# Kernel optimization log

Measured on AMD Instinct MI355X. Metric: run time of the kernel, lower is better.

The kernel has to match this reference:

```python
import jax, jax.numpy as jnp
import numpy as np

N, E, G, DIN, DH = 50000, 800000, 256, 128, 128
BN_EPS = 1e-5


def _gin_layer(h, src, dst, W1, b1, gamma, beta, W2, b2):
    # GINConv (eps=0): agg_i = sum_{(j->i) in edges} h_j ; z = agg + h
    agg = jnp.zeros_like(h).at[dst].add(h[src])
    z = agg + h
    z = z @ W1 + b1
    # BatchNorm1d (training mode: batch stats over nodes, biased var)
    mean = z.mean(axis=0)
    var = z.var(axis=0)
    z = gamma * (z - mean) * jax.lax.rsqrt(var + BN_EPS) + beta
    z = jax.nn.relu(z)
    z = z @ W2 + b2
    return jax.nn.relu(z)


def setup_inputs() -> dict:
    key = jax.random.key(0)
    ks = jax.random.split(key, 12)
    x = jax.random.normal(ks[0], (N, DIN), dtype=jnp.float32)
    edge_index = jax.random.randint(ks[1], (2, E), 0, N, dtype=jnp.int32)
    batch = jnp.sort(jax.random.randint(ks[2], (N,), 0, G, dtype=jnp.int32))
    s = 0.05
    W1 = jax.random.normal(ks[3], (7, DIN, DH), dtype=jnp.float32) * s
    b1 = jnp.zeros((7, DH), dtype=jnp.float32)
    gamma = jnp.ones((7, DH), dtype=jnp.float32)
    beta = jnp.zeros((7, DH), dtype=jnp.float32)
    W2 = jax.random.normal(ks[4], (7, DH, DH), dtype=jnp.float32) * s
    b2 = jnp.zeros((7, DH), dtype=jnp.float32)
    Wl1 = jax.random.normal(ks[5], (14 * DH, 14 * DH), dtype=jnp.float32) * s
    bl1 = jnp.zeros((14 * DH,), dtype=jnp.float32)
    Wl2 = jax.random.normal(ks[6], (14 * DH, 1), dtype=jnp.float32) * s
    bl2 = jnp.zeros((1,), dtype=jnp.float32)
    return {"x": x, "edge_index": edge_index, "batch": batch,
            "W1": W1, "b1": b1, "gamma": gamma, "beta": beta,
            "W2": W2, "b2": b2, "Wl1": Wl1, "bl1": bl1,
            "Wl2": Wl2, "bl2": bl2}


def reference(x, edge_index, batch, W1, b1, gamma, beta, W2, b2, Wl1, bl1, Wl2, bl2):
    src, dst = edge_index[0], edge_index[1]
    hs = []
    h = x
    for i in range(7):
        h = _gin_layer(h, src, dst, W1[i], b1[i], gamma[i], beta[i], W2[i], b2[i])
        hs.append(h)
    adds = [jax.ops.segment_sum(hi, batch, num_segments=G) for hi in hs]
    maxs = [jax.ops.segment_max(hi, batch, num_segments=G) for hi in hs]
    h = jnp.concatenate(adds + maxs, axis=1)  # [G, 14*DH]
    h = jax.nn.relu(h @ Wl1 + bl1)
    h = h @ Wl2 + bl2
    return (jax.nn.sigmoid(h), h)
```

## Files before the change

### kernel.cpp

```cpp
#include <hip/hip_runtime.h>
#include <cstdint>
#include <cstddef>

#define NN 50000
#define NE 800000
#define NG 256
#define NLAY 7
#define NBLK 782
#define CAP 18432

typedef float f32x4 __attribute__((ext_vector_type(4)));
typedef __bf16 bf16x8 __attribute__((ext_vector_type(8)));
typedef _Float16 h16x8 __attribute__((ext_vector_type(8)));

__device__ __forceinline__ float4 ld4(const float* p) { return *(const float4*)p; }
__device__ __forceinline__ void addh8(float4& x, float4& y, h16x8 v) {
  x.x += (float)v[0]; x.y += (float)v[1]; x.z += (float)v[2]; x.w += (float)v[3];
  y.x += (float)v[4]; y.y += (float)v[5]; y.z += (float)v[6]; y.w += (float)v[7];
}

__global__ void k_init(const float* __restrict__ x, const float* __restrict__ W1,
                       const float* __restrict__ W2, int* __restrict__ counts,
                       int* __restrict__ gcur, float* __restrict__ pooled,
                       _Float16* __restrict__ hb,
                       __bf16* __restrict__ w1f, __bf16* __restrict__ w2f) {
  int i = blockIdx.x * 256 + threadIdx.x;
  if (i < NN) counts[i] = 0;
  if (i < 49) gcur[i] = i * CAP;
  if (i < NG * 1792) pooled[i] = 0.f;
  if (i < NN * 128) hb[i] = (_Float16)x[i];
  if (i < NLAY * 32768) {
    int l = i >> 15, pos = i & 32767;
    int j = pos & 7, ln = (pos >> 3) & 63, slot = (pos >> 9) & 15, kc = pos >> 13;
    int hl = slot & 1, ctp = (slot >> 1) & 3, hfp = slot >> 3;
    int n = hfp * 64 + ctp * 16 + (ln & 15);
    int k = kc * 32 + ((ln >> 4) << 3) + j;
    float a = W1[l * 16384 + k * 128 + n];
    float b = W2[l * 16384 + k * 128 + n];
    __bf16 ah = (__bf16)a, bh = (__bf16)b;
    w1f[i] = hl ? (__bf16)(a - (float)ah) : ah;
    w2f[i] = hl ? (__bf16)(b - (float)bh) : bh;
  }
}

__global__ void k_hist(const int* __restrict__ edge, int* __restrict__ counts) {
  int e = blockIdx.x * 256 + threadIdx.x;
  if (e < NE) atomicAdd(&counts[edge[NE + e]], 1);
}

__global__ void k_part(const int* __restrict__ counts, int* __restrict__ bsum) {
  __shared__ int sm[256];
  int b = blockIdx.x, t = threadIdx.x;
  int i = b * 256 + t;
  sm[t] = (i < NN) ? counts[i] : 0;
  __syncthreads();
  for (int s = 128; s > 0; s >>= 1) {
    if (t < s) sm[t] += sm[t + s];
    __syncthreads();
  }
  if (t == 0) bsum[b] = sm[0];
}

__global__ void k_bscan(const int* __restrict__ bsum, int* __restrict__ boff,
                        int* __restrict__ row_ptr) {
  __shared__ int sm[256];
  int t = threadIdx.x;
  int v = (t < 196) ? bsum[t] : 0;
  sm[t] = v;
  __syncthreads();
  int val = v;
  for (int off = 1; off < 256; off <<= 1) {
    int o = (t >= off) ? sm[t - off] : 0;
    __syncthreads();
    val += o;
    sm[t] = val;
    __syncthreads();
  }
  if (t < 196) boff[t] = val - v;
  if (t == 255) row_ptr[NN] = val;
}

__global__ void k_rowptr(const int* __restrict__ counts, const int* __restrict__ boff,
                         int* __restrict__ row_ptr) {
  __shared__ int sm[256];
  int b = blockIdx.x, t = threadIdx.x;
  int i = b * 256 + t;
  int c = (i < NN) ? counts[i] : 0;
  sm[t] = c;
  __syncthreads();
  int val = c;
  for (int off = 1; off < 256; off <<= 1) {
    int o = (t >= off) ? sm[t - off] : 0;
    __syncthreads();
    val += o;
    sm[t] = val;
    __syncthreads();
  }
  if (i < NN) row_ptr[i] = val - c + boff[b];
}

__global__ __launch_bounds__(256) void k_binA(const int* __restrict__ edge,
                                              int* __restrict__ gcur,
                                              unsigned int* __restrict__ bins) {
  __shared__ int lh[49], lbase[49], lt[49];
  const int tid = threadIdx.x;
  const int e0 = blockIdx.x * 3125, e1 = e0 + 3125;
  if (tid < 49) { lh[tid] = 0; lt[tid] = 0; }
  __syncthreads();
  for (int e = e0 + tid; e < e1; e += 256)
    atomicAdd(&lh[edge[NE + e] >> 10], 1);
  __syncthreads();
  if (tid < 49) lbase[tid] = atomicAdd(&gcur[tid], lh[tid]);
  __syncthreads();
  for (int e = e0 + tid; e < e1; e += 256) {
    int dst = edge[NE + e], src = edge[e];
    int r = dst >> 10;
    int t = atomicAdd(&lt[r], 1);
    bins[lbase[r] + t] = ((unsigned)dst << 16) | (unsigned)src;
  }
}

__global__ __launch_bounds__(512) void k_binB(const int* __restrict__ row_ptr,
                                              const int* __restrict__ gcur,
                                              const unsigned int* __restrict__ bins,
                                              unsigned short* __restrict__ csr16) {
  __shared__ int lcur[1024];
  __shared__ unsigned short lcsr[24576];
  const int blk = blockIdx.x, tid = threadIdx.x;
  const int base = blk << 10;
  const int nn = (base + 1024 <= NN) ? 1024 : (NN - base);
  const int seg0 = row_ptr[base];
  const int seg1 = row_ptr[(base + 1024 <= NN) ? (base + 1024) : NN];
  for (int i = tid; i < nn; i += 512) lcur[i] = row_ptr[base + i] - seg0;
  __syncthreads();
  const int tot = gcur[blk] - blk * CAP;
  for (int t = tid; t < tot; t += 512) {
    unsigned int p = bins[blk * CAP + t];
    int dst = (int)(p >> 16), src = (int)(p & 0xffffu);
    int pos = atomicAdd(&lcur[dst - base], 1);
    lcsr[pos] = (unsigned short)src;
  }
  __syncthreads();
  for (int i = tid; i < seg1 - seg0; i += 512) csr16[seg0 + i] = lcsr[i];
}

__device__ __forceinline__ void split8(const float4 v0, const float4 v1,
                                       bf16x8& hi, bf16x8& lo) {
  float f[8] = {v0.x, v0.y, v0.z, v0.w, v1.x, v1.y, v1.z, v1.w};
  #pragma unroll
  for (int j = 0; j < 8; ++j) {
    __bf16 h = (__bf16)f[j];
    hi[j] = h;
    lo[j] = (__bf16)(f[j] - (float)h);
  }
}

__device__ __forceinline__ void mfma_phase(
    int tid, const __bf16* __restrict__ wf, float (*zs)[132], f32x4 acc[4])
{
  const int wv = tid >> 6, stripe = wv >> 1, half = wv & 1;
  const int lane = tid & 63, q = lane >> 4, m = lane & 15;
  #pragma unroll
  for (int kc = 0; kc < 4; ++kc) {
    const int k0 = kc * 32 + q * 8;
    float4 v0 = *(const float4*)&zs[stripe * 16 + m][k0];
    float4 v1 = *(const float4*)&zs[stripe * 16 + m][k0 + 4];
    bf16x8 ah, al;
    split8(v0, v1, ah, al);
    #pragma unroll
    for (int ct = 0; ct < 4; ++ct) {
      const int sbase = (half * 4 + ct) * 2;
      const __bf16* bp = wf + (((size_t)(kc * 16 + sbase) * 64 + lane) << 3);
      bf16x8 bh = *(const bf16x8*)bp;
      bf16x8 bl = *(const bf16x8*)(bp + 512);
      acc[ct] = __builtin_amdgcn_mfma_f32_16x16x32_bf16(ah, bh, acc[ct], 0, 0, 0);
      acc[ct] = __builtin_amdgcn_mfma_f32_16x16x32_bf16(ah, bl, acc[ct], 0, 0, 0);
      acc[ct] = __builtin_amdgcn_mfma_f32_16x16x32_bf16(al, bh, acc[ct], 0, 0, 0);
    }
  }
  __syncthreads();
}

__global__ __launch_bounds__(512) void k_fused1(
    const _Float16* __restrict__ hb, const int* __restrict__ row_ptr,
    const unsigned short* __restrict__ csr_src, const __bf16* __restrict__ wf,
    const float* __restrict__ bias, _Float16* __restrict__ zb,
    float* __restrict__ psum, float* __restrict__ psq)
{
  __shared__ float zs[64][132];
  const int tid = threadIdx.x;
  const int m0 = blockIdx.x * 64;

  {
    const int lr = tid >> 3;
    const int sub = tid & 7;
    const int r = m0 + lr;
    const int c0 = sub << 4;
    float4 a0 = make_float4(0,0,0,0), a1 = a0, a2 = a0, a3 = a0;
    float4 b0 = a0, b1 = a0, b2 = a0, b3 = a0;
    if (r < NN) {
      const _Float16* hp = hb + ((size_t)r << 7) + c0;
      addh8(a0, a1, *(const h16x8*)hp);
      addh8(a2, a3, *(const h16x8*)(hp + 8));
      int e = row_ptr[r], e1 = row_ptr[r + 1];
      for (; e + 3 < e1; e += 4) {
        const _Float16* p0 = hb + ((size_t)csr_src[e] << 7) + c0;
        const _Float16* p1 = hb + ((size_t)csr_src[e + 1] << 7) + c0;
        const _Float16* p2 = hb + ((size_t)csr_src[e + 2] << 7) + c0;
        const _Float16* p3 = hb + ((size_t)csr_src[e + 3] << 7) + c0;
        h16x8 v0a = *(const h16x8*)p0, v0b = *(const h16x8*)(p0 + 8);
        h16x8 v1a = *(const h16x8*)p1, v1b = *(const h16x8*)(p1 + 8);
        h16x8 v2a = *(const h16x8*)p2, v2b = *(const h16x8*)(p2 + 8);
        h16x8 v3a = *(const h16x8*)p3, v3b = *(const h16x8*)(p3 + 8);
        addh8(a0, a1, v0a); addh8(a2, a3, v0b);
        addh8(b0, b1, v1a); addh8(b2, b3, v1b);
        addh8(a0, a1, v2a); addh8(a2, a3, v2b);
        addh8(b0, b1, v3a); addh8(b2, b3, v3b);
      }
      for (; e < e1; ++e) {
        const _Float16* p0 = hb + ((size_t)csr_src[e] << 7) + c0;
        addh8(a0, a1, *(const h16x8*)p0);
        addh8(a2, a3, *(const h16x8*)(p0 + 8));
      }
      a0.x += b0.x; a0.y += b0.y; a0.z += b0.z; a0.w += b0.w;
      a1.x += b1.x; a1.y += b1.y; a1.z += b1.z; a1.w += b1.w;
      a2.x += b2.x; a2.y += b2.y; a2.z += b2.z; a2.w += b2.w;
      a3.x += b3.x; a3.y += b3.y; a3.z += b3.z; a3.w += b3.w;
    }
    *(float4*)&zs[lr][c0 + 0] = a0;
    *(float4*)&zs[lr][c0 + 4] = a1;
    *(float4*)&zs[lr][c0 + 8] = a2;
    *(float4*)&zs[lr][c0 + 12] = a3;
  }
  __syncthreads();

  const int wv = tid >> 6, stripe = wv >> 1, half = wv & 1;
  const int lane = tid & 63, q = lane >> 4, m = lane & 15;
  f32x4 acc[4] = {};
  mfma_phase(tid, wf, zs, acc);

  float* red_s = (float*)zs;
  float* red_q = red_s + 2176;
  const int sl = stripe * 4 + q;
  #pragma unroll
  for (int ct = 0; ct < 4; ++ct) {
    const int col = half * 64 + ct * 16 + m;
    const float bb = bias[col];
    float s = 0.f, qq = 0.f;
    #pragma unroll
    for (int i = 0; i < 4; ++i) {
      int r = m0 + stripe * 16 + q * 4 + i;
      if (r < NN) {
        float o = acc[ct][i] + bb;
        zb[((size_t)r << 7) + col] = (_Float16)o;
        s += o; qq += o * o;
      }
    }
    red_s[col * 17 + sl] = s;
    red_q[col * 17 + sl] = qq;
  }
  __syncthreads();
  if (tid < 128) {
    float s = 0.f, qq = 0.f;
    #pragma unroll
    for (int k = 0; k < 16; ++k) {
      s += red_s[tid * 17 + k];
      qq += red_q[tid * 17 + k];
    }
    psum[blockIdx.x * 128 + tid] = s;
    psq[blockIdx.x * 128 + tid] = qq;
  }
}

__global__ __launch_bounds__(256) void k_bnfin(
    const float* __restrict__ psum, const float* __restrict__ psq,
    const float* __restrict__ gamma, const float* __restrict__ beta,
    float* __restrict__ ab) {
  __shared__ float ss[256], sq[256];
  int col = blockIdx.x;
  int t = threadIdx.x;
  float s = 0.f, q = 0.f;
  for (int b = t; b < NBLK; b += 256) {
    s += psum[b * 128 + col];
    q += psq[b * 128 + col];
  }
  ss[t] = s; sq[t] = q;
  __syncthreads();
  for (int st = 128; st > 0; st >>= 1) {
    if (t < st) { ss[t] += ss[t + st]; sq[t] += sq[t + st]; }
    __syncthreads();
  }
  if (t == 0) {
    float mean = ss[0] * (1.f / NN);
    float var = sq[0] * (1.f / NN) - mean * mean;
    float rstd = rsqrtf(var + 1e-5f);
    float a = gamma[col] * rstd;
    ab[col] = a;
    ab[128 + col] = beta[col] - mean * a;
  }
}

__global__ __launch_bounds__(512) void k_fused2(
    const _Float16* __restrict__ zb, const float* __restrict__ ab,
    const __bf16* __restrict__ wf, const float* __restrict__ bias,
    _Float16* __restrict__ hb, const int* __restrict__ batch,
    float* __restrict__ pooled, int layer)
{
  __shared__ float zs[64][132];
  const int tid = threadIdx.x;
  const int m0 = blockIdx.x * 64;

  {
    const int lr = tid >> 3;
    const int sub = tid & 7;
    const int r = m0 + lr;
    const int c0 = sub << 4;
    h16x8 u0 = {}, u1 = {};
    if (r < NN) {
      const _Float16* rp = zb + ((size_t)r << 7) + c0;
      u0 = *(const h16x8*)rp;
      u1 = *(const h16x8*)(rp + 8);
    }
    float4 v0 = make_float4((float)u0[0], (float)u0[1], (float)u0[2], (float)u0[3]);
    float4 v1 = make_float4((float)u0[4], (float)u0[5], (float)u0[6], (float)u0[7]);
    float4 v2 = make_float4((float)u1[0], (float)u1[1], (float)u1[2], (float)u1[3]);
    float4 v3 = make_float4((float)u1[4], (float)u1[5], (float)u1[6], (float)u1[7]);
    float4 s0 = ld4(ab + c0), s1 = ld4(ab + c0 + 4);
    float4 s2 = ld4(ab + c0 + 8), s3 = ld4(ab + c0 + 12);
    float4 o0 = ld4(ab + 128 + c0), o1 = ld4(ab + 128 + c0 + 4);
    float4 o2 = ld4(ab + 128 + c0 + 8), o3 = ld4(ab + 128 + c0 + 12);
    float4 y0, y1, y2, y3;
    y0.x = fmaxf(fmaf(s0.x, v0.x, o0.x), 0.f); y0.y = fmaxf(fmaf(s0.y, v0.y, o0.y), 0.f);
    y0.z = fmaxf(fmaf(s0.z, v0.z, o0.z), 0.f); y0.w = fmaxf(fmaf(s0.w, v0.w, o0.w), 0.f);
    y1.x = fmaxf(fmaf(s1.x, v1.x, o1.x), 0.f); y1.y = fmaxf(fmaf(s1.y, v1.y, o1.y), 0.f);
    y1.z = fmaxf(fmaf(s1.z, v1.z, o1.z), 0.f); y1.w = fmaxf(fmaf(s1.w, v1.w, o1.w), 0.f);
    y2.x = fmaxf(fmaf(s2.x, v2.x, o2.x), 0.f); y2.y = fmaxf(fmaf(s2.y, v2.y, o2.y), 0.f);
    y2.z = fmaxf(fmaf(s2.z, v2.z, o2.z), 0.f); y2.w = fmaxf(fmaf(s2.w, v2.w, o2.w), 0.f);
    y3.x = fmaxf(fmaf(s3.x, v3.x, o3.x), 0.f); y3.y = fmaxf(fmaf(s3.y, v3.y, o3.y), 0.f);
    y3.z = fmaxf(fmaf(s3.z, v3.z, o3.z), 0.f); y3.w = fmaxf(fmaf(s3.w, v3.w, o3.w), 0.f);
    *(float4*)&zs[lr][c0 + 0] = y0;
    *(float4*)&zs[lr][c0 + 4] = y1;
    *(float4*)&zs[lr][c0 + 8] = y2;
    *(float4*)&zs[lr][c0 + 12] = y3;
  }
  __syncthreads();

  const int wv = tid >> 6, stripe = wv >> 1, half = wv & 1;
  const int lane = tid & 63, q = lane >> 4, m = lane & 15;
  f32x4 acc[4] = {};
  mfma_phase(tid, wf, zs, acc);

  int bg[4];
  #pragma unroll
  for (int i = 0; i < 4; ++i) {
    int r = m0 + stripe * 16 + q * 4 + i;
    bg[i] = (r < NN) ? batch[r] : -1;
  }
  #pragma unroll
  for (int ct = 0; ct < 4; ++ct) {
    const int col = half * 64 + ct * 16 + m;
    const float bb = bias[col];
    #pragma unroll
    for (int i = 0; i < 4; ++i) {
      int r = m0 + stripe * 16 + q * 4 + i;
      float v = fmaxf(acc[ct][i] + bb, 0.f);
      acc[ct][i] = v;
      if (r < NN) hb[((size_t)r << 7) + col] = (_Float16)v;
    }
  }

  int gstart = batch[m0];
  int gend = batch[(m0 + 63 < NN) ? (m0 + 63) : (NN - 1)];
  float* red_s = (float*)zs;
  float* red_m = red_s + 2176;
  const int sl = stripe * 4 + q;
  for (int g = gstart; g <= gend; ++g) {
    __syncthreads();
    #pragma unroll
    for (int ct = 0; ct < 4; ++ct) {
      const int col = half * 64 + ct * 16 + m;
      float s = 0.f, mx = 0.f;
      #pragma unroll
      for (int i = 0; i < 4; ++i) {
        if (bg[i] == g) { s += acc[ct][i]; mx = fmaxf(mx, acc[ct][i]); }
      }
      red_s[col * 17 + sl] = s;
      red_m[col * 17 + sl] = mx;
    }
    __syncthreads();
    if (tid < 128) {
      float s = 0.f, mx = 0.f;
      #pragma unroll
      for (int k = 0; k < 16; ++k) {
        s += red_s[tid * 17 + k];
        mx = fmaxf(mx, red_m[tid * 17 + k]);
      }
      if (s != 0.f) atomicAdd(&pooled[g * 1792 + layer * 128 + tid], s);
      if (mx != 0.f)
        atomicMax((int*)&pooled[g * 1792 + 896 + layer * 128 + tid], __float_as_int(mx));
    }
  }
}

__global__ __launch_bounds__(256) void k_wl1prep(
    const float* __restrict__ Wl1, __bf16* __restrict__ wh, __bf16* __restrict__ wl) {
  __shared__ float tile[32][33];
  const int k0 = blockIdx.x * 32, n0 = blockIdx.y * 32;
  const int lr = threadIdx.x >> 5, lc = threadIdx.x & 31;
  #pragma unroll
  for (int it = 0; it < 4; ++it) {
    int rr = lr + it * 8;
    tile[rr][lc] = Wl1[(size_t)(k0 + rr) * 1792 + n0 + lc];
  }
  __syncthreads();
  #pragma unroll
  for (int it = 0; it < 4; ++it) {
    int rr = lr + it * 8;
    float v = tile[lc][rr];
    __bf16 h = (__bf16)v;
    wh[(size_t)(n0 + rr) * 1792 + k0 + lc] = h;
    wl[(size_t)(n0 + rr) * 1792 + k0 + lc] = (__bf16)(v - (float)h);
  }
}

__global__ __launch_bounds__(256) void k_mlp1a(
    const float* __restrict__ P, const __bf16* __restrict__ wh,
    const __bf16* __restrict__ wl, float* __restrict__ part)
{
  const int tid = threadIdx.x;
  const int n0 = blockIdx.x * 64;
  const int m0 = blockIdx.y * 64;
  const int kc = blockIdx.z;
  const int kbase = kc * 448;
  const int w = tid >> 6, lane = tid & 63, q = lane >> 4, m = lane & 15;
  const int row = m0 + w * 16 + m;
  f32x4 acc[4] = {};
  const float* rp = P + (size_t)row * 1792;
  #pragma unroll 2
  for (int ks = 0; ks < 14; ++ks) {
    const int k0 = kbase + ks * 32 + q * 8;
    float4 v0 = ld4(rp + k0), v1 = ld4(rp + k0 + 4);
    bf16x8 ah, al;
    split8(v0, v1, ah, al);
    #pragma unroll
    for (int ct = 0; ct < 4; ++ct) {
      const int n = n0 + ct * 16 + m;
      bf16x8 bh = *(const bf16x8*)(wh + (size_t)n * 1792 + k0);
      bf16x8 bl = *(const bf16x8*)(wl + (size_t)n * 1792 + k0);
      acc[ct] = __builtin_amdgcn_mfma_f32_16x16x32_bf16(ah, bh, acc[ct], 0, 0, 0);
      acc[ct] = __builtin_amdgcn_mfma_f32_16x16x32_bf16(ah, bl, acc[ct], 0, 0, 0);
      acc[ct] = __builtin_amdgcn_mfma_f32_16x16x32_bf16(al, bh, acc[ct], 0, 0, 0);
    }
  }
  float* pp = part + (size_t)kc * 458752;
  #pragma unroll
  for (int ct = 0; ct < 4; ++ct) {
    const int n = n0 + ct * 16 + m;
    #pragma unroll
    for (int i = 0; i < 4; ++i) {
      int r = m0 + w * 16 + q * 4 + i;
      pp[(size_t)r * 1792 + n] = acc[ct][i];
    }
  }
}

__global__ void k_mlp2(const float* __restrict__ part, const float* __restrict__ bl1,
                       const float* __restrict__ Wl2, const float* __restrict__ bl2,
                       float* __restrict__ out) {
  __shared__ float red[256];
  int g = blockIdx.x, t = threadIdx.x;
  float p = 0.f;
  for (int k = t; k < 1792; k += 256) {
    size_t idx = (size_t)g * 1792 + k;
    float s = bl1[k];
    #pragma unroll
    for (int kc = 0; kc < 4; ++kc) s += part[(size_t)kc * 458752 + idx];
    p += fmaxf(s, 0.f) * Wl2[k];
  }
  red[t] = p;
  __syncthreads();
  for (int s = 128; s > 0; s >>= 1) {
    if (t < s) red[t] += red[t + s];
    __syncthreads();
  }
  if (t == 0) {
    float l = red[0] + bl2[0];
    out[g] = 1.f / (1.f + expf(-l));
    out[NG + g] = l;
  }
}

extern "C" void kernel_launch(void* const* d_in, const int* in_sizes, int n_in,
                              void* d_out, int out_size, void* d_ws, size_t ws_size,
                              hipStream_t stream) {
  const float* x     = (const float*)d_in[0];
  const int*   edge  = (const int*)d_in[1];
  const int*   batch = (const int*)d_in[2];
  const float* W1    = (const float*)d_in[3];
  const float* b1    = (const float*)d_in[4];
  const float* gamma = (const float*)d_in[5];
  const float* beta  = (const float*)d_in[6];
  const float* W2    = (const float*)d_in[7];
  const float* b2    = (const float*)d_in[8];
  const float* Wl1   = (const float*)d_in[9];
  const float* bl1   = (const float*)d_in[10];
  const float* Wl2   = (const float*)d_in[11];
  const float* bl2   = (const float*)d_in[12];
  float* out = (float*)d_out;

  int* wsi = (int*)d_ws;
  int* row_ptr = wsi;
  int* counts  = wsi + 50048;
  int* bsum    = wsi + 100096;
  int* boff    = wsi + 100352;
  int* gcur    = wsi + 100608;
  unsigned short* csr16 = (unsigned short*)(wsi + 100864);
  float* wsf   = (float*)(wsi + 950912);
  _Float16* zb     = (_Float16*)wsf;
  _Float16* hb     = (_Float16*)(wsf + 6400000);
  float*    part   = wsf + 9600000;
  float*    psum   = wsf + 12800000;
  float*    psq    = wsf + 12900096;
  float*    ab     = wsf + 13000192;
  float*    pooled = wsf + 13000448;
  __bf16*   w1f    = (__bf16*)(wsf + 13459200);
  __bf16*   w2f    = (__bf16*)(wsf + 13573888);
  unsigned int* bins = (unsigned int*)wsf;
  __bf16*   wl1h   = (__bf16*)wsf;
  __bf16*   wl1l   = (__bf16*)(wsf + 1605632);

  k_init<<<25000, 256, 0, stream>>>(x, W1, W2, counts, gcur, pooled, hb, w1f, w2f);
  k_hist<<<3125, 256, 0, stream>>>(edge, counts);
  k_part<<<196, 256, 0, stream>>>(counts, bsum);
  k_bscan<<<1, 256, 0, stream>>>(bsum, boff, row_ptr);
  k_rowptr<<<196, 256, 0, stream>>>(counts, boff, row_ptr);
  k_binA<<<256, 256, 0, stream>>>(edge, gcur, bins);
  k_binB<<<49, 512, 0, stream>>>(row_ptr, gcur, bins, csr16);

  for (int i = 0; i < NLAY; ++i) {
    k_fused1<<<NBLK, 512, 0, stream>>>(hb, row_ptr, csr16, w1f + i * 32768,
                                       b1 + i * 128, zb, psum, psq);
    k_bnfin<<<128, 256, 0, stream>>>(psum, psq, gamma + i * 128, beta + i * 128, ab);
    k_fused2<<<NBLK, 512, 0, stream>>>(zb, ab, w2f + i * 32768,
                                       b2 + i * 128, hb, batch, pooled, i);
  }
  k_wl1prep<<<dim3(56, 56), 256, 0, stream>>>(Wl1, wl1h, wl1l);
  k_mlp1a<<<dim3(28, 4, 4), 256, 0, stream>>>(pooled, wl1h, wl1l, part);
  k_mlp2<<<256, 256, 0, stream>>>(part, bl1, Wl2, bl2, out);
}
```

Measured before the change: 710.9 us.

## Halve fused1 row tile to 32 and sum neighbor rows in fp16 pairs

The first fused GIN kernel now handles 32 rows per block instead of 64, launching twice as many blocks. Each thread gathers 8 columns instead of 16, and each wave computes two MFMA column tiles instead of four. The neighbor gather is unrolled to 8 edges, with the 8 rows summed pairwise in fp16 before conversion to fp32. Occupancy is raised through a launch-bounds hint and smaller LDS use, and the psum/psq partial buffers are moved and resized for the larger block count. The fp16 pairwise accumulation trades fewer conversions for reduced precision in the aggregation, and weight fragments are reloaded by more waves.

```diff
diff --git a/kernel.cpp b/kernel.cpp
--- a/kernel.cpp
+++ b/kernel.cpp
@@ -7,6 +7,7 @@
 #define NG 256
 #define NLAY 7
 #define NBLK 782
+#define NBLK1 1563
 #define CAP 18432
 
 typedef float f32x4 __attribute__((ext_vector_type(4)));
@@ -181,69 +182,77 @@
   __syncthreads();
 }
 
-__global__ __launch_bounds__(512) void k_fused1(
+__global__ __launch_bounds__(512, 8) void k_fused1(
     const _Float16* __restrict__ hb, const int* __restrict__ row_ptr,
     const unsigned short* __restrict__ csr_src, const __bf16* __restrict__ wf,
     const float* __restrict__ bias, _Float16* __restrict__ zb,
     float* __restrict__ psum, float* __restrict__ psq)
 {
-  __shared__ float zs[64][132];
+  __shared__ float zs[32][132];
   const int tid = threadIdx.x;
-  const int m0 = blockIdx.x * 64;
+  const int m0 = blockIdx.x * 32;
 
   {
-    const int lr = tid >> 3;
-    const int sub = tid & 7;
+    const int lr = tid >> 4;
+    const int sub = tid & 15;
     const int r = m0 + lr;
-    const int c0 = sub << 4;
-    float4 a0 = make_float4(0,0,0,0), a1 = a0, a2 = a0, a3 = a0;
-    float4 b0 = a0, b1 = a0, b2 = a0, b3 = a0;
+    const int c0 = sub << 3;
+    float4 a0 = make_float4(0.f, 0.f, 0.f, 0.f), a1 = a0;
     if (r < NN) {
-      const _Float16* hp = hb + ((size_t)r << 7) + c0;
-      addh8(a0, a1, *(const h16x8*)hp);
-      addh8(a2, a3, *(const h16x8*)(hp + 8));
+      addh8(a0, a1, *(const h16x8*)(hb + ((size_t)r << 7) + c0));
       int e = row_ptr[r], e1 = row_ptr[r + 1];
-      for (; e + 3 < e1; e += 4) {
-        const _Float16* p0 = hb + ((size_t)csr_src[e] << 7) + c0;
-        const _Float16* p1 = hb + ((size_t)csr_src[e + 1] << 7) + c0;
-        const _Float16* p2 = hb + ((size_t)csr_src[e + 2] << 7) + c0;
-        const _Float16* p3 = hb + ((size_t)csr_src[e + 3] << 7) + c0;
-        h16x8 v0a = *(const h16x8*)p0, v0b = *(const h16x8*)(p0 + 8);
-        h16x8 v1a = *(const h16x8*)p1, v1b = *(const h16x8*)(p1 + 8);
-        h16x8 v2a = *(const h16x8*)p2, v2b = *(const h16x8*)(p2 + 8);
-        h16x8 v3a = *(const h16x8*)p3, v3b = *(const h16x8*)(p3 + 8);
-        addh8(a0, a1, v0a); addh8(a2, a3, v0b);
-        addh8(b0, b1, v1a); addh8(b2, b3, v1b);
-        addh8(a0, a1, v2a); addh8(a2, a3, v2b);
-        addh8(b0, b1, v3a); addh8(b2, b3, v3b);
+      for (; e + 7 < e1; e += 8) {
+        const h16x8 v0 = *(const h16x8*)(hb + ((size_t)csr_src[e + 0] << 7) + c0);
+        const h16x8 v1 = *(const h16x8*)(hb + ((size_t)csr_src[e + 1] << 7) + c0);
+        const h16x8 v2 = *(const h16x8*)(hb + ((size_t)csr_src[e + 2] << 7) + c0);
+        const h16x8 v3 = *(const h16x8*)(hb + ((size_t)csr_src[e + 3] << 7) + c0);
+        const h16x8 v4 = *(const h16x8*)(hb + ((size_t)csr_src[e + 4] << 7) + c0);
+        const h16x8 v5 = *(const h16x8*)(hb + ((size_t)csr_src[e + 5] << 7) + c0);
+        const h16x8 v6 = *(const h16x8*)(hb + ((size_t)csr_src[e + 6] << 7) + c0);
+        const h16x8 v7 = *(const h16x8*)(hb + ((size_t)csr_src[e + 7] << 7) + c0);
+        h16x8 t0 = v0 + v1, t1 = v2 + v3, t2 = v4 + v5, t3 = v6 + v7;
+        h16x8 u0 = t0 + t1, u1 = t2 + t3;
+        addh8(a0, a1, u0 + u1);
       }
-      for (; e < e1; ++e) {
-        const _Float16* p0 = hb + ((size_t)csr_src[e] << 7) + c0;
-        addh8(a0, a1, *(const h16x8*)p0);
-        addh8(a2, a3, *(const h16x8*)(p0 + 8));
-      }
-      a0.x += b0.x; a0.y += b0.y; a0.z += b0.z; a0.w += b0.w;
-      a1.x += b1.x; a1.y += b1.y; a1.z += b1.z; a1.w += b1.w;
-      a2.x += b2.x; a2.y += b2.y; a2.z += b2.z; a2.w += b2.w;
-      a3.x += b3.x; a3.y += b3.y; a3.z += b3.z; a3.w += b3.w;
+      for (; e < e1; ++e)
+        addh8(a0, a1, *(const h16x8*)(hb + ((size_t)csr_src[e] << 7) + c0));
     }
     *(float4*)&zs[lr][c0 + 0] = a0;
     *(float4*)&zs[lr][c0 + 4] = a1;
-    *(float4*)&zs[lr][c0 + 8] = a2;
-    *(float4*)&zs[lr][c0 + 12] = a3;
-  }
-  __syncthreads();
-
-  const int wv = tid >> 6, stripe = wv >> 1, half = wv & 1;
+  }
+  __syncthreads();
+
+  const int wv = tid >> 6;
+  const int stripe = wv >> 2, half = (wv >> 1) & 1, cpair = wv & 1;
   const int lane = tid & 63, q = lane >> 4, m = lane & 15;
-  f32x4 acc[4] = {};
-  mfma_phase(tid, wf, zs, acc);
+  f32x4 acc[2] = {};
+  #pragma unroll
+  for (int kc = 0; kc < 4; ++kc) {
+    const int k0 = kc * 32 + q * 8;
+    float4 v0 = *(const float4*)&zs[stripe * 16 + m][k0];
+    float4 v1 = *(const float4*)&zs[stripe * 16 + m][k0 + 4];
+    bf16x8 ah, al;
+    split8(v0, v1, ah, al);
+    #pragma unroll
+    for (int j = 0; j < 2; ++j) {
+      const int ct = cpair * 2 + j;
+      const int sbase = (half * 4 + ct) * 2;
+      const __bf16* bp = wf + (((size_t)(kc * 16 + sbase) * 64 + lane) << 3);
+      bf16x8 bh = *(const bf16x8*)bp;
+      bf16x8 bl = *(const bf16x8*)(bp + 512);
+      acc[j] = __builtin_amdgcn_mfma_f32_16x16x32_bf16(ah, bh, acc[j], 0, 0, 0);
+      acc[j] = __builtin_amdgcn_mfma_f32_16x16x32_bf16(ah, bl, acc[j], 0, 0, 0);
+      acc[j] = __builtin_amdgcn_mfma_f32_16x16x32_bf16(al, bh, acc[j], 0, 0, 0);
+    }
+  }
+  __syncthreads();
 
   float* red_s = (float*)zs;
-  float* red_q = red_s + 2176;
+  float* red_q = red_s + 1152;
   const int sl = stripe * 4 + q;
   #pragma unroll
-  for (int ct = 0; ct < 4; ++ct) {
+  for (int j = 0; j < 2; ++j) {
+    const int ct = cpair * 2 + j;
     const int col = half * 64 + ct * 16 + m;
     const float bb = bias[col];
     float s = 0.f, qq = 0.f;
@@ -251,21 +260,21 @@
     for (int i = 0; i < 4; ++i) {
       int r = m0 + stripe * 16 + q * 4 + i;
       if (r < NN) {
-        float o = acc[ct][i] + bb;
+        float o = acc[j][i] + bb;
         zb[((size_t)r << 7) + col] = (_Float16)o;
         s += o; qq += o * o;
       }
     }
-    red_s[col * 17 + sl] = s;
-    red_q[col * 17 + sl] = qq;
+    red_s[col * 9 + sl] = s;
+    red_q[col * 9 + sl] = qq;
   }
   __syncthreads();
   if (tid < 128) {
     float s = 0.f, qq = 0.f;
     #pragma unroll
-    for (int k = 0; k < 16; ++k) {
-      s += red_s[tid * 17 + k];
-      qq += red_q[tid * 17 + k];
+    for (int k = 0; k < 8; ++k) {
+      s += red_s[tid * 9 + k];
+      qq += red_q[tid * 9 + k];
     }
     psum[blockIdx.x * 128 + tid] = s;
     psq[blockIdx.x * 128 + tid] = qq;
@@ -280,7 +289,7 @@
   int col = blockIdx.x;
   int t = threadIdx.x;
   float s = 0.f, q = 0.f;
-  for (int b = t; b < NBLK; b += 256) {
+  for (int b = t; b < NBLK1; b += 256) {
     s += psum[b * 128 + col];
     q += psq[b * 128 + col];
   }
@@ -519,8 +528,8 @@
   _Float16* zb     = (_Float16*)wsf;
   _Float16* hb     = (_Float16*)(wsf + 6400000);
   float*    part   = wsf + 9600000;
-  float*    psum   = wsf + 12800000;
-  float*    psq    = wsf + 12900096;
+  float*    psum   = wsf + 9600000;
+  float*    psq    = wsf + 9800192;
   float*    ab     = wsf + 13000192;
   float*    pooled = wsf + 13000448;
   __bf16*   w1f    = (__bf16*)(wsf + 13459200);
@@ -538,8 +547,8 @@
   k_binB<<<49, 512, 0, stream>>>(row_ptr, gcur, bins, csr16);
 
   for (int i = 0; i < NLAY; ++i) {
-    k_fused1<<<NBLK, 512, 0, stream>>>(hb, row_ptr, csr16, w1f + i * 32768,
-                                       b1 + i * 128, zb, psum, psq);
+    k_fused1<<<NBLK1, 512, 0, stream>>>(hb, row_ptr, csr16, w1f + i * 32768,
+                                        b1 + i * 128, zb, psum, psq);
     k_bnfin<<<128, 256, 0, stream>>>(psum, psq, gamma + i * 128, beta + i * 128, ab);
     k_fused2<<<NBLK, 512, 0, stream>>>(zb, ab, w2f + i * 32768,
                                        b2 + i * 128, hb, batch, pooled, i);
```

After: 683.1 us. 3.9% less time.
